# Kernel optimization log

Measured on AMD Instinct MI355X. Metric: run time of the kernel, lower is better.

## Reference

```python
import jax, jax.numpy as jnp
import numpy as np

SIGMA = 0.1
B = 1.0
EPS = 1e-5


def setup_inputs() -> dict:
    key = jax.random.key(0)
    k1, k2 = jax.random.split(key)
    featureT = jax.random.normal(k1, (2, 256, 64, 64), dtype=jnp.float32)
    featureI = jax.random.normal(k2, (2, 256, 64, 64), dtype=jnp.float32)
    return {"featureT": featureT, "featureI": featureI}


def reference(featureT, featureI):
    # NCHW -> NHWC
    fI = jnp.transpose(featureI, (0, 2, 3, 1))
    fT = jnp.transpose(featureT, (0, 2, 3, 1))
    # center both by target mean over N, H, W (shape [1,1,1,C])
    meanT = fT.mean(axis=(0, 1, 2), keepdims=True)
    fI = fI - meanT
    fT = fT - meanT
    # channelwise L2 normalize
    fI = fI / jnp.linalg.norm(fI, axis=3, keepdims=True)
    fT = fT / jnp.linalg.norm(fT, axis=3, keepdims=True)
    N, H, W, C = fT.shape
    P = H * W
    # conv2d with 1x1 target patches == cosine similarity vs every target patch
    Tp = fT.reshape(N, P, C)                       # [N, P, C]
    dist = jnp.einsum('nhwc,npc->nhwp', fI, Tp)    # [N, H, W, P]
    raw_dist = (1.0 - dist) / 2.0
    # relative distance: divide by min over target-patch axis
    rel = raw_dist / (jnp.min(raw_dist, axis=3, keepdims=True) + EPS)
    # exp weighting, normalized over target-patch axis
    Wt = jnp.exp((B - rel) / SIGMA)
    CX = Wt / Wt.sum(axis=3, keepdims=True)        # [N, H, W, P]
    # max over spatial (query) dims, mean over target patches, -log, mean
    CX = CX.max(axis=2).max(axis=1)                # [N, P]
    CX = -jnp.log(CX.mean(axis=1))                 # [N]
    return jnp.mean(CX)
```

## Files before the change

### kernel.cpp

```cpp
#include <hip/hip_runtime.h>
#include <hip/hip_bf16.h>
#include <math.h>

#define NB 2
#define C 256
#define P 4096
#define EPS_F 1e-5f

typedef __attribute__((ext_vector_type(8))) short short8;
typedef __attribute__((ext_vector_type(4))) float f32x4;

__device__ __forceinline__ float bf2f(unsigned short u) {
    union { unsigned int i; float f; } x;
    x.i = ((unsigned int)u) << 16;
    return x.f;
}

__global__ void k_mean(const float* __restrict__ fT, float* __restrict__ mean) {
    int c = blockIdx.x;
    int t = threadIdx.x;
    const float* p0 = fT + (size_t)c * P;
    const float* p1 = fT + (size_t)(C + c) * P;
    float s = 0.f;
    for (int i = t; i < P; i += 256) s += p0[i] + p1[i];
    __shared__ float red[256];
    red[t] = s; __syncthreads();
    for (int o = 128; o > 0; o >>= 1) { if (t < o) red[t] += red[t + o]; __syncthreads(); }
    if (t == 0) mean[c] = red[0] * (1.f / 8192.f);
}

__global__ __launch_bounds__(256) void k_normpack(const float* __restrict__ f,
                                                  const float* __restrict__ mean,
                                                  __hip_bfloat16* __restrict__ out) {
    __shared__ float mn[C];
    __shared__ float tile[C][33];
    __shared__ float part[8][32];
    __shared__ float srn[32];
    int t = threadIdx.x;
    mn[t] = mean[t];
    __syncthreads();
    int n = blockIdx.y, p0 = blockIdx.x * 32;
    int pl = t & 31, cg = t >> 5;
    const float* base = f + (size_t)n * C * P + p0 + pl;
    float acc = 0.f;
    #pragma unroll 4
    for (int cc = 0; cc < 32; cc++) {
        int c = cg * 32 + cc;
        float v = base[(size_t)c * P] - mn[c];
        tile[c][pl] = v;
        acc += v * v;
    }
    part[cg][pl] = acc;
    __syncthreads();
    if (t < 32) {
        float s = 0.f;
        #pragma unroll
        for (int g = 0; g < 8; g++) s += part[g][t];
        srn[t] = rsqrtf(s);
    }
    __syncthreads();
    #pragma unroll
    for (int it = 0; it < 4; it++) {
        int flat = it * 2048 + t * 8;
        int p = flat >> 8;
        int c = flat & 255;
        float rn = srn[p];
        union { __hip_bfloat16 h[8]; short8 s; } u;
        #pragma unroll
        for (int k = 0; k < 8; k++)
            u.h[k] = __float2bfloat16(tile[c + k][p] * rn);
        *(short8*)(out + ((size_t)(n * P + p0 + p)) * C + c) = u.s;
    }
}

__device__ __forceinline__ void stage_tile(const __hip_bfloat16* __restrict__ gbase,
                                           __hip_bfloat16* lbuf, int kk, int wid, int lane) {
    #pragma unroll
    for (int j = 0; j < 2; j++) {
        int row = wid * 32 + j * 16 + (lane >> 2);
        int cb = (lane & 3) * 16;
        int scb = cb ^ (((row >> 1) & 3) << 4);
        const char* gp = (const char*)gbase + (size_t)row * (C * 2) + kk * 64 + scb;
        char* lp = (char*)lbuf + (wid * 32 + j * 16) * 64;
        __builtin_amdgcn_global_load_lds(
            (const __attribute__((address_space(1))) void*)gp,
            (__attribute__((address_space(3))) void*)lp, 16, 0, 0);
    }
}

__device__ __forceinline__ short8 ldfrag(const __hip_bfloat16* lbuf, int rloc, int kb) {
    int addr = rloc * 64 + (kb ^ (((rloc >> 1) & 3) << 4));
    return *(const short8*)((const char*)lbuf + addr);
}

__global__ __launch_bounds__(256) void k_gemm(const __hip_bfloat16* __restrict__ TI,
                                              const __hip_bfloat16* __restrict__ TT,
                                              __hip_bfloat16* __restrict__ D,
                                              float* __restrict__ Mpart) {
    __shared__ char smem[49152];
    int lane = threadIdx.x & 63, wid = threadIdx.x >> 6;
    int wr = wid >> 1, wc = wid & 1;
    int n = blockIdx.z;
    const __hip_bfloat16* A = TI + ((size_t)n * P + blockIdx.y * 128) * C;
    const __hip_bfloat16* B = TT + ((size_t)n * P + blockIdx.x * 128) * C;

    f32x4 acc[4][4];
    #pragma unroll
    for (int m = 0; m < 4; m++)
        #pragma unroll
        for (int nt = 0; nt < 4; nt++)
            acc[m][nt] = (f32x4){0.f, 0.f, 0.f, 0.f};

    int rA = lane & 15;
    int kb = (lane >> 4) * 16;

    stage_tile(A, (__hip_bfloat16*)(smem), 0, wid, lane);
    stage_tile(B, (__hip_bfloat16*)(smem + 24576), 0, wid, lane);
    stage_tile(A, (__hip_bfloat16*)(smem + 8192), 1, wid, lane);
    stage_tile(B, (__hip_bfloat16*)(smem + 24576 + 8192), 1, wid, lane);
    asm volatile("s_waitcnt vmcnt(4)" ::: "memory");
    __builtin_amdgcn_s_barrier();
    __builtin_amdgcn_sched_barrier(0);

    #pragma unroll
    for (int t = 0; t < 8; t++) {
        int cur = t % 3;
        if (t < 6) {
            int nxt = (t + 2) % 3;
            stage_tile(A, (__hip_bfloat16*)(smem + nxt * 8192), t + 2, wid, lane);
            stage_tile(B, (__hip_bfloat16*)(smem + 24576 + nxt * 8192), t + 2, wid, lane);
        }
        __hip_bfloat16* lAc = (__hip_bfloat16*)(smem + cur * 8192);
        __hip_bfloat16* lBc = (__hip_bfloat16*)(smem + 24576 + cur * 8192);
        short8 a[4], b[4];
        #pragma unroll
        for (int m = 0; m < 4; m++)
            a[m] = ldfrag(lAc, wr * 64 + m * 16 + rA, kb);
        #pragma unroll
        for (int nt = 0; nt < 4; nt++)
            b[nt] = ldfrag(lBc, wc * 64 + nt * 16 + rA, kb);
        #pragma unroll
        for (int m = 0; m < 4; m++)
            #pragma unroll
            for (int nt = 0; nt < 4; nt++)
                acc[m][nt] = __builtin_amdgcn_mfma_f32_16x16x32_bf16(a[m], b[nt], acc[m][nt], 0, 0, 0);
        if (t < 6)       asm volatile("s_waitcnt vmcnt(4)" ::: "memory");
        else if (t == 6) asm volatile("s_waitcnt vmcnt(0)" ::: "memory");
        __builtin_amdgcn_s_barrier();
        __builtin_amdgcn_sched_barrier(0);
    }

    int rj = (lane >> 4) * 4, cl = lane & 15;
    {
        char* tb = smem;
        #pragma unroll
        for (int m = 0; m < 4; m++)
            #pragma unroll
            for (int nt = 0; nt < 4; nt++)
                #pragma unroll
                for (int j = 0; j < 4; j++) {
                    int row = wr * 64 + m * 16 + rj + j;
                    int colb = (wc * 64 + nt * 16 + cl) * 2;
                    *(__hip_bfloat16*)(tb + row * 256 + (colb ^ (((row >> 2) & 3) << 5))) =
                        __float2bfloat16(acc[m][nt][j]);
                }
        __syncthreads();
        int qb0 = blockIdx.y * 128, pb0 = blockIdx.x * 128;
        char* Dn = (char*)(D + (size_t)n * P * P);
        #pragma unroll
        for (int rb = 0; rb < 8; rb++) {
            int row = wid * 32 + rb * 4 + (lane >> 4);
            int sb = cl * 16;
            short8 v = *(const short8*)(tb + row * 256 + (sb ^ (((row >> 2) & 3) << 5)));
            *(short8*)(Dn + ((size_t)(qb0 + row) * P + pb0) * 2 + sb) = v;
        }
    }

    int qb = blockIdx.y * 128 + wr * 64;
    int pt = blockIdx.x * 2 + wc;
    #pragma unroll
    for (int m = 0; m < 4; m++) {
        f32x4 mx = acc[m][0];
        #pragma unroll
        for (int nt = 1; nt < 4; nt++)
            #pragma unroll
            for (int j = 0; j < 4; j++)
                mx[j] = fmaxf(mx[j], acc[m][nt][j]);
        #pragma unroll
        for (int j = 0; j < 4; j++)
            #pragma unroll
            for (int o = 1; o < 16; o <<= 1)
                mx[j] = fmaxf(mx[j], __shfl_xor(mx[j], o));
        if ((lane & 15) == 0) {
            int qbase = qb + m * 16 + (lane >> 4) * 4;
            #pragma unroll
            for (int j = 0; j < 4; j++)
                Mpart[((size_t)(n * P + qbase + j)) * 64 + pt] = mx[j];
        }
    }
}

__global__ __launch_bounds__(512) void k_zcol(const __hip_bfloat16* __restrict__ D,
                                              const float* __restrict__ Mpart,
                                              float* __restrict__ Cpart) {
    __shared__ __hip_bfloat16 tile[8][P];
    __shared__ float st2[8], sc[8];
    int t = threadIdx.x, lane = t & 63, wv = t >> 6;
    int n = blockIdx.y, g = blockIdx.x;
    int q = g * 8 + wv;
    size_t row = (size_t)n * P + q;

    const char* gsrc = (const char*)(D + row * P);
    char* ldst = (char*)&tile[wv][0];
    #pragma unroll
    for (int i = 0; i < 8; i++)
        __builtin_amdgcn_global_load_lds(
            (const __attribute__((address_space(1))) void*)(gsrc + i * 1024 + lane * 16),
            (__attribute__((address_space(3))) void*)(ldst + i * 1024), 16, 0, 0);

    float m = Mpart[row * 64 + lane];
    #pragma unroll
    for (int o = 32; o > 0; o >>= 1) m = fmaxf(m, __shfl_xor(m, o));
    float t2 = 5.f / ((1.f - m) * 0.5f + EPS_F);

    __syncthreads();

    const short8* trow = (const short8*)&tile[wv][0];
    float z = 0.f;
    #pragma unroll
    for (int k = 0; k < 8; k++) {
        short8 v = trow[k * 64 + lane];
        #pragma unroll
        for (int j = 0; j < 8; j++)
            z += __expf(t2 * (bf2f((unsigned short)v[j]) - m));
    }
    #pragma unroll
    for (int o = 32; o > 0; o >>= 1) z += __shfl_xor(z, o);
    if (lane == 0) { st2[wv] = t2; sc[wv] = -t2 * m - logf(z); }
    __syncthreads();

    float cm[8];
    #pragma unroll
    for (int j = 0; j < 8; j++) cm[j] = -1e30f;
    #pragma unroll
    for (int r = 0; r < 8; r++) {
        short8 v = *(const short8*)&tile[r][t * 8];
        float tt = st2[r], cc = sc[r];
        #pragma unroll
        for (int j = 0; j < 8; j++)
            cm[j] = fmaxf(cm[j], fmaf(tt, bf2f((unsigned short)v[j]), cc));
    }
    float* cp = Cpart + ((size_t)(n * 512 + g)) * P + t * 8;
    f32x4 v0 = {cm[0], cm[1], cm[2], cm[3]};
    f32x4 v1 = {cm[4], cm[5], cm[6], cm[7]};
    *(f32x4*)cp = v0;
    *(f32x4*)(cp + 4) = v1;
}

__global__ void k_colred1(const float* __restrict__ Cpart, float* __restrict__ Cred2) {
    int np = blockIdx.x * 256 + threadIdx.x;
    int n = np >> 12, p = np & 4095;
    const float* base = Cpart + (size_t)(n * 512) * P + p;
    float c = -1e30f;
    int g0 = blockIdx.y * 64;
    #pragma unroll 8
    for (int g = 0; g < 64; g++)
        c = fmaxf(c, base[(size_t)(g0 + g) * P]);
    Cred2[blockIdx.y * 8192 + np] = c;
}

__global__ void k_colred2(const float* __restrict__ Cred2, float* __restrict__ colmax) {
    int np = blockIdx.x * 256 + threadIdx.x;
    float c = -1e30f;
    #pragma unroll
    for (int y = 0; y < 8; y++)
        c = fmaxf(c, Cred2[y * 8192 + np]);
    colmax[np] = __expf(c);
}

__global__ void k_final(const float* __restrict__ colmax, float* __restrict__ out) {
    __shared__ float red[256];
    int t = threadIdx.x;
    float cx[NB];
    for (int n = 0; n < NB; n++) {
        float s = 0.f;
        for (int i = t; i < P; i += 256) s += colmax[n * P + i];
        red[t] = s; __syncthreads();
        for (int o = 128; o > 0; o >>= 1) { if (t < o) red[t] += red[t + o]; __syncthreads(); }
        cx[n] = -logf(red[0] * (1.f / (float)P));
        __syncthreads();
    }
    if (t == 0) out[0] = 0.5f * (cx[0] + cx[1]);
}

extern "C" void kernel_launch(void* const* d_in, const int* in_sizes, int n_in,
                              void* d_out, int out_size, void* d_ws, size_t ws_size,
                              hipStream_t stream) {
    const float* fT = (const float*)d_in[0];
    const float* fI = (const float*)d_in[1];
    float* out = (float*)d_out;

    char* ws = (char*)d_ws;
    size_t off = 0;
    __hip_bfloat16* TI = (__hip_bfloat16*)(ws + off); off += 4194304;
    __hip_bfloat16* TT = (__hip_bfloat16*)(ws + off); off += 4194304;
    __hip_bfloat16* D  = (__hip_bfloat16*)(ws + off); off += (size_t)NB * P * P * 2;
    float* Mpart  = (float*)(ws + off); off += (size_t)NB * P * 64 * 4;
    float* Cpart  = (float*)(ws + off); off += (size_t)NB * 512 * P * 4;
    float* Cred2  = (float*)(ws + off); off += (size_t)8 * NB * P * 4;
    float* mean   = (float*)(ws + off); off += 1024;
    float* colmax = (float*)(ws + off); off += 32768;

    k_mean<<<256, 256, 0, stream>>>(fT, mean);
    k_normpack<<<dim3(128, 2), 256, 0, stream>>>(fI, mean, TI);
    k_normpack<<<dim3(128, 2), 256, 0, stream>>>(fT, mean, TT);
    k_gemm<<<dim3(32, 32, 2), 256, 0, stream>>>(TI, TT, D, Mpart);
    k_zcol<<<dim3(512, 2), 512, 0, stream>>>(D, Mpart, Cpart);
    k_colred1<<<dim3(32, 8), 256, 0, stream>>>(Cpart, Cred2);
    k_colred2<<<32, 256, 0, stream>>>(Cred2, colmax);
    k_final<<<1, 256, 0, stream>>>(colmax, out);
}
```

Before: 96.67 us.

## Fuse column-max reduction into zcol via order-preserving atomicMax

```diff
diff --git a/kernel.cpp b/kernel.cpp
--- a/kernel.cpp
+++ b/kernel.cpp
@@ -14,6 +14,14 @@
     union { unsigned int i; float f; } x;
     x.i = ((unsigned int)u) << 16;
     return x.f;
+}
+
+__device__ __forceinline__ unsigned enc(float f) {
+    unsigned u = __float_as_uint(f);
+    return (u & 0x80000000u) ? ~u : (u | 0x80000000u);
+}
+__device__ __forceinline__ float dec(unsigned k) {
+    return (k & 0x80000000u) ? __uint_as_float(k & 0x7FFFFFFFu) : __uint_as_float(~k);
 }
 
 __global__ void k_mean(const float* __restrict__ fT, float* __restrict__ mean) {
@@ -202,89 +210,73 @@
 
 __global__ __launch_bounds__(512) void k_zcol(const __hip_bfloat16* __restrict__ D,
                                               const float* __restrict__ Mpart,
-                                              float* __restrict__ Cpart) {
+                                              unsigned int* __restrict__ colmax) {
     __shared__ __hip_bfloat16 tile[8][P];
     __shared__ float st2[8], sc[8];
     int t = threadIdx.x, lane = t & 63, wv = t >> 6;
     int n = blockIdx.y, g = blockIdx.x;
-    int q = g * 8 + wv;
-    size_t row = (size_t)n * P + q;
-
-    const char* gsrc = (const char*)(D + row * P);
-    char* ldst = (char*)&tile[wv][0];
-    #pragma unroll
-    for (int i = 0; i < 8; i++)
-        __builtin_amdgcn_global_load_lds(
-            (const __attribute__((address_space(1))) void*)(gsrc + i * 1024 + lane * 16),
-            (__attribute__((address_space(3))) void*)(ldst + i * 1024), 16, 0, 0);
-
-    float m = Mpart[row * 64 + lane];
-    #pragma unroll
-    for (int o = 32; o > 0; o >>= 1) m = fmaxf(m, __shfl_xor(m, o));
-    float t2 = 5.f / ((1.f - m) * 0.5f + EPS_F);
-
-    __syncthreads();
-
-    const short8* trow = (const short8*)&tile[wv][0];
-    float z = 0.f;
-    #pragma unroll
-    for (int k = 0; k < 8; k++) {
-        short8 v = trow[k * 64 + lane];
-        #pragma unroll
-        for (int j = 0; j < 8; j++)
-            z += __expf(t2 * (bf2f((unsigned short)v[j]) - m));
-    }
-    #pragma unroll
-    for (int o = 32; o > 0; o >>= 1) z += __shfl_xor(z, o);
-    if (lane == 0) { st2[wv] = t2; sc[wv] = -t2 * m - logf(z); }
-    __syncthreads();
 
     float cm[8];
     #pragma unroll
     for (int j = 0; j < 8; j++) cm[j] = -1e30f;
-    #pragma unroll
-    for (int r = 0; r < 8; r++) {
-        short8 v = *(const short8*)&tile[r][t * 8];
-        float tt = st2[r], cc = sc[r];
-        #pragma unroll
-        for (int j = 0; j < 8; j++)
-            cm[j] = fmaxf(cm[j], fmaf(tt, bf2f((unsigned short)v[j]), cc));
-    }
-    float* cp = Cpart + ((size_t)(n * 512 + g)) * P + t * 8;
-    f32x4 v0 = {cm[0], cm[1], cm[2], cm[3]};
-    f32x4 v1 = {cm[4], cm[5], cm[6], cm[7]};
-    *(f32x4*)cp = v0;
-    *(f32x4*)(cp + 4) = v1;
-}
-
-__global__ void k_colred1(const float* __restrict__ Cpart, float* __restrict__ Cred2) {
-    int np = blockIdx.x * 256 + threadIdx.x;
-    int n = np >> 12, p = np & 4095;
-    const float* base = Cpart + (size_t)(n * 512) * P + p;
-    float c = -1e30f;
-    int g0 = blockIdx.y * 64;
-    #pragma unroll 8
-    for (int g = 0; g < 64; g++)
-        c = fmaxf(c, base[(size_t)(g0 + g) * P]);
-    Cred2[blockIdx.y * 8192 + np] = c;
-}
-
-__global__ void k_colred2(const float* __restrict__ Cred2, float* __restrict__ colmax) {
-    int np = blockIdx.x * 256 + threadIdx.x;
-    float c = -1e30f;
-    #pragma unroll
-    for (int y = 0; y < 8; y++)
-        c = fmaxf(c, Cred2[y * 8192 + np]);
-    colmax[np] = __expf(c);
-}
-
-__global__ void k_final(const float* __restrict__ colmax, float* __restrict__ out) {
+
+    #pragma unroll
+    for (int s = 0; s < 2; s++) {
+        int q = g * 16 + s * 8 + wv;
+        size_t row = (size_t)n * P + q;
+        const char* gsrc = (const char*)(D + row * P);
+        char* ldst = (char*)&tile[wv][0];
+        #pragma unroll
+        for (int i = 0; i < 8; i++)
+            __builtin_amdgcn_global_load_lds(
+                (const __attribute__((address_space(1))) void*)(gsrc + i * 1024 + lane * 16),
+                (__attribute__((address_space(3))) void*)(ldst + i * 1024), 16, 0, 0);
+
+        float m = Mpart[row * 64 + lane];
+        #pragma unroll
+        for (int o = 32; o > 0; o >>= 1) m = fmaxf(m, __shfl_xor(m, o));
+        float t2 = 5.f / ((1.f - m) * 0.5f + EPS_F);
+
+        __syncthreads();
+
+        const short8* trow = (const short8*)&tile[wv][0];
+        float z = 0.f;
+        #pragma unroll
+        for (int k = 0; k < 8; k++) {
+            short8 v = trow[k * 64 + lane];
+            #pragma unroll
+            for (int j = 0; j < 8; j++)
+                z += __expf(t2 * (bf2f((unsigned short)v[j]) - m));
+        }
+        #pragma unroll
+        for (int o = 32; o > 0; o >>= 1) z += __shfl_xor(z, o);
+        if (lane == 0) { st2[wv] = t2; sc[wv] = -t2 * m - logf(z); }
+        __syncthreads();
+
+        #pragma unroll
+        for (int r = 0; r < 8; r++) {
+            short8 v = *(const short8*)&tile[r][t * 8];
+            float tt = st2[r], cc = sc[r];
+            #pragma unroll
+            for (int j = 0; j < 8; j++)
+                cm[j] = fmaxf(cm[j], fmaf(tt, bf2f((unsigned short)v[j]), cc));
+        }
+        __syncthreads();
+    }
+
+    unsigned int* cp = colmax + (size_t)n * P + t * 8;
+    #pragma unroll
+    for (int j = 0; j < 8; j++)
+        atomicMax(&cp[j], enc(cm[j]));
+}
+
+__global__ void k_final(const unsigned int* __restrict__ colmax, float* __restrict__ out) {
     __shared__ float red[256];
     int t = threadIdx.x;
     float cx[NB];
     for (int n = 0; n < NB; n++) {
         float s = 0.f;
-        for (int i = t; i < P; i += 256) s += colmax[n * P + i];
+        for (int i = t; i < P; i += 256) s += __expf(dec(colmax[n * P + i]));
         red[t] = s; __syncthreads();
         for (int o = 128; o > 0; o >>= 1) { if (t < o) red[t] += red[t + o]; __syncthreads(); }
         cx[n] = -logf(red[0] * (1.f / (float)P));
@@ -306,17 +298,15 @@
     __hip_bfloat16* TT = (__hip_bfloat16*)(ws + off); off += 4194304;
     __hip_bfloat16* D  = (__hip_bfloat16*)(ws + off); off += (size_t)NB * P * P * 2;
     float* Mpart  = (float*)(ws + off); off += (size_t)NB * P * 64 * 4;
-    float* Cpart  = (float*)(ws + off); off += (size_t)NB * 512 * P * 4;
-    float* Cred2  = (float*)(ws + off); off += (size_t)8 * NB * P * 4;
     float* mean   = (float*)(ws + off); off += 1024;
-    float* colmax = (float*)(ws + off); off += 32768;
+    unsigned int* colmax = (unsigned int*)(ws + off); off += 32768;
+
+    hipMemsetAsync(colmax, 0, NB * P * sizeof(unsigned int), stream);
 
     k_mean<<<256, 256, 0, stream>>>(fT, mean);
     k_normpack<<<dim3(128, 2), 256, 0, stream>>>(fI, mean, TI);
     k_normpack<<<dim3(128, 2), 256, 0, stream>>>(fT, mean, TT);
     k_gemm<<<dim3(32, 32, 2), 256, 0, stream>>>(TI, TT, D, Mpart);
-    k_zcol<<<dim3(512, 2), 512, 0, stream>>>(D, Mpart, Cpart);
-    k_colred1<<<dim3(32, 8), 256, 0, stream>>>(Cpart, Cred2);
-    k_colred2<<<32, 256, 0, stream>>>(Cred2, colmax);
+    k_zcol<<<dim3(256, 2), 512, 0, stream>>>(D, Mpart, colmax);
     k_final<<<1, 256, 0, stream>>>(colmax, out);
 }
```

Result: slower. 161.6 us (+67.1%).

## Merge normpack launches, process two row groups per zcol block, single-pass column reduction

Applied to the files above, without the earlier changes.

```diff
diff --git a/kernel.cpp b/kernel.cpp
--- a/kernel.cpp
+++ b/kernel.cpp
@@ -29,14 +29,18 @@
     if (t == 0) mean[c] = red[0] * (1.f / 8192.f);
 }
 
-__global__ __launch_bounds__(256) void k_normpack(const float* __restrict__ f,
+__global__ __launch_bounds__(256) void k_normpack(const float* __restrict__ fI,
+                                                  const float* __restrict__ fT,
                                                   const float* __restrict__ mean,
-                                                  __hip_bfloat16* __restrict__ out) {
+                                                  __hip_bfloat16* __restrict__ TI,
+                                                  __hip_bfloat16* __restrict__ TT) {
     __shared__ float mn[C];
     __shared__ float tile[C][33];
     __shared__ float part[8][32];
     __shared__ float srn[32];
     int t = threadIdx.x;
+    const float* f = blockIdx.z ? fT : fI;
+    __hip_bfloat16* out = blockIdx.z ? TT : TI;
     mn[t] = mean[t];
     __syncthreads();
     int n = blockIdx.y, p0 = blockIdx.x * 32;
@@ -207,74 +211,70 @@
     __shared__ float st2[8], sc[8];
     int t = threadIdx.x, lane = t & 63, wv = t >> 6;
     int n = blockIdx.y, g = blockIdx.x;
-    int q = g * 8 + wv;
-    size_t row = (size_t)n * P + q;
-
-    const char* gsrc = (const char*)(D + row * P);
-    char* ldst = (char*)&tile[wv][0];
-    #pragma unroll
-    for (int i = 0; i < 8; i++)
-        __builtin_amdgcn_global_load_lds(
-            (const __attribute__((address_space(1))) void*)(gsrc + i * 1024 + lane * 16),
-            (__attribute__((address_space(3))) void*)(ldst + i * 1024), 16, 0, 0);
-
-    float m = Mpart[row * 64 + lane];
-    #pragma unroll
-    for (int o = 32; o > 0; o >>= 1) m = fmaxf(m, __shfl_xor(m, o));
-    float t2 = 5.f / ((1.f - m) * 0.5f + EPS_F);
-
-    __syncthreads();
-
-    const short8* trow = (const short8*)&tile[wv][0];
-    float z = 0.f;
-    #pragma unroll
-    for (int k = 0; k < 8; k++) {
-        short8 v = trow[k * 64 + lane];
-        #pragma unroll
-        for (int j = 0; j < 8; j++)
-            z += __expf(t2 * (bf2f((unsigned short)v[j]) - m));
-    }
-    #pragma unroll
-    for (int o = 32; o > 0; o >>= 1) z += __shfl_xor(z, o);
-    if (lane == 0) { st2[wv] = t2; sc[wv] = -t2 * m - logf(z); }
-    __syncthreads();
 
     float cm[8];
     #pragma unroll
     for (int j = 0; j < 8; j++) cm[j] = -1e30f;
-    #pragma unroll
-    for (int r = 0; r < 8; r++) {
-        short8 v = *(const short8*)&tile[r][t * 8];
-        float tt = st2[r], cc = sc[r];
-        #pragma unroll
-        for (int j = 0; j < 8; j++)
-            cm[j] = fmaxf(cm[j], fmaf(tt, bf2f((unsigned short)v[j]), cc));
-    }
-    float* cp = Cpart + ((size_t)(n * 512 + g)) * P + t * 8;
+
+    #pragma unroll
+    for (int s = 0; s < 2; s++) {
+        int q = g * 16 + s * 8 + wv;
+        size_t row = (size_t)n * P + q;
+        const char* gsrc = (const char*)(D + row * P);
+        char* ldst = (char*)&tile[wv][0];
+        #pragma unroll
+        for (int i = 0; i < 8; i++)
+            __builtin_amdgcn_global_load_lds(
+                (const __attribute__((address_space(1))) void*)(gsrc + i * 1024 + lane * 16),
+                (__attribute__((address_space(3))) void*)(ldst + i * 1024), 16, 0, 0);
+
+        float m = Mpart[row * 64 + lane];
+        #pragma unroll
+        for (int o = 32; o > 0; o >>= 1) m = fmaxf(m, __shfl_xor(m, o));
+        float t2 = 5.f / ((1.f - m) * 0.5f + EPS_F);
+
+        __syncthreads();
+
+        const short8* trow = (const short8*)&tile[wv][0];
+        float z = 0.f;
+        #pragma unroll
+        for (int k = 0; k < 8; k++) {
+            short8 v = trow[k * 64 + lane];
+            #pragma unroll
+            for (int j = 0; j < 8; j++)
+                z += __expf(t2 * (bf2f((unsigned short)v[j]) - m));
+        }
+        #pragma unroll
+        for (int o = 32; o > 0; o >>= 1) z += __shfl_xor(z, o);
+        if (lane == 0) { st2[wv] = t2; sc[wv] = -t2 * m - logf(z); }
+        __syncthreads();
+
+        #pragma unroll
+        for (int r = 0; r < 8; r++) {
+            short8 v = *(const short8*)&tile[r][t * 8];
+            float tt = st2[r], cc = sc[r];
+            #pragma unroll
+            for (int j = 0; j < 8; j++)
+                cm[j] = fmaxf(cm[j], fmaf(tt, bf2f((unsigned short)v[j]), cc));
+        }
+        __syncthreads();
+    }
+
+    float* cp = Cpart + ((size_t)(n * 256 + g)) * P + t * 8;
     f32x4 v0 = {cm[0], cm[1], cm[2], cm[3]};
     f32x4 v1 = {cm[4], cm[5], cm[6], cm[7]};
     *(f32x4*)cp = v0;
     *(f32x4*)(cp + 4) = v1;
 }
 
-__global__ void k_colred1(const float* __restrict__ Cpart, float* __restrict__ Cred2) {
+__global__ void k_colred(const float* __restrict__ Cpart, float* __restrict__ colmax) {
     int np = blockIdx.x * 256 + threadIdx.x;
     int n = np >> 12, p = np & 4095;
-    const float* base = Cpart + (size_t)(n * 512) * P + p;
+    const float* base = Cpart + (size_t)(n * 256) * P + p;
     float c = -1e30f;
-    int g0 = blockIdx.y * 64;
     #pragma unroll 8
-    for (int g = 0; g < 64; g++)
-        c = fmaxf(c, base[(size_t)(g0 + g) * P]);
-    Cred2[blockIdx.y * 8192 + np] = c;
-}
-
-__global__ void k_colred2(const float* __restrict__ Cred2, float* __restrict__ colmax) {
-    int np = blockIdx.x * 256 + threadIdx.x;
-    float c = -1e30f;
-    #pragma unroll
-    for (int y = 0; y < 8; y++)
-        c = fmaxf(c, Cred2[y * 8192 + np]);
+    for (int g = 0; g < 256; g++)
+        c = fmaxf(c, base[(size_t)g * P]);
     colmax[np] = __expf(c);
 }
 
@@ -306,17 +306,14 @@
     __hip_bfloat16* TT = (__hip_bfloat16*)(ws + off); off += 4194304;
     __hip_bfloat16* D  = (__hip_bfloat16*)(ws + off); off += (size_t)NB * P * P * 2;
     float* Mpart  = (float*)(ws + off); off += (size_t)NB * P * 64 * 4;
-    float* Cpart  = (float*)(ws + off); off += (size_t)NB * 512 * P * 4;
-    float* Cred2  = (float*)(ws + off); off += (size_t)8 * NB * P * 4;
+    float* Cpart  = (float*)(ws + off); off += (size_t)NB * 256 * P * 4;
     float* mean   = (float*)(ws + off); off += 1024;
     float* colmax = (float*)(ws + off); off += 32768;
 
     k_mean<<<256, 256, 0, stream>>>(fT, mean);
-    k_normpack<<<dim3(128, 2), 256, 0, stream>>>(fI, mean, TI);
-    k_normpack<<<dim3(128, 2), 256, 0, stream>>>(fT, mean, TT);
+    k_normpack<<<dim3(128, 2, 2), 256, 0, stream>>>(fI, fT, mean, TI, TT);
     k_gemm<<<dim3(32, 32, 2), 256, 0, stream>>>(TI, TT, D, Mpart);
-    k_zcol<<<dim3(512, 2), 512, 0, stream>>>(D, Mpart, Cpart);
-    k_colred1<<<dim3(32, 8), 256, 0, stream>>>(Cpart, Cred2);
-    k_colred2<<<32, 256, 0, stream>>>(Cred2, colmax);
+    k_zcol<<<dim3(256, 2), 512, 0, stream>>>(D, Mpart, Cpart);
+    k_colred<<<32, 256, 0, stream>>>(Cpart, colmax);
     k_final<<<1, 256, 0, stream>>>(colmax, out);
 }
```

Result: slower. 116.7 us (+20.7%).
